# Optimization experiments

Measured on AMD Instinct MI355X. Metric: run time of the kernel, lower is better.

The kernel has to match this reference:

```python
import jax, jax.numpy as jnp
import numpy as np

T, B, N, C, H, D = 4, 8, 1024, 512, 8, 64
EPS = 1e-5


def setup_inputs() -> dict:
    key = jax.random.key(0)
    ks = jax.random.split(key, 16)
    d = {"x": jax.random.normal(ks[0], (T, B, N, C), jnp.float32)}
    for i, nm in enumerate(["q", "k", "v", "p"]):
        kW, kmu, kvar = jax.random.split(ks[1 + i], 3)
        d[f"W{nm}"] = jax.random.normal(kW, (C, C), jnp.float32) * 0.02
        d[f"b{nm}"] = jnp.zeros((C,), jnp.float32)
        d[f"g{nm}"] = jnp.ones((C,), jnp.float32)
        d[f"beta{nm}"] = jnp.zeros((C,), jnp.float32)
        d[f"mu{nm}"] = jax.random.normal(kmu, (C,), jnp.float32) * 0.1
        d[f"var{nm}"] = jax.random.uniform(kvar, (C,), jnp.float32, 0.5, 1.5)
    return d


def _lin_bn(z, W, b, g, beta, mu, var):
    # nn.Linear over channel dim, then eval-mode BatchNorm1d per channel
    y = jnp.einsum('tbnc,dc->tbnd', z, W) + b
    return (y - mu) * (g * jax.lax.rsqrt(var + EPS)) + beta


def _to_heads(z):
    # (t,b,n,c) -> (t,b,h,n,d)
    return z.reshape(T, B, N, H, D).transpose(0, 1, 3, 2, 4)


def reference(x, Wq, bq, gq, betaq, muq, varq,
              Wk, bk, gk, betak, muk, vark,
              Wv, bv, gv, betav, muv, varv,
              Wp, bp, gp, betap, mup, varp):
    q = _to_heads(_lin_bn(x, Wq, bq, gq, betaq, muq, varq))
    k = _to_heads(_lin_bn(x, Wk, bk, gk, betak, muk, vark))
    v = _to_heads(_lin_bn(x, Wv, bv, gv, betav, muv, varv))
    # attention_linear variant: kv = (k^T @ v) / N ; y = q @ kv
    kv = jnp.einsum('tbhnd,tbhne->tbhde', k, v) / float(N)  # (t,b,h,d,d)
    y = jnp.einsum('tbhnd,tbhde->tbhne', q, kv)             # (t,b,h,n,d)
    y = y.transpose(0, 1, 3, 2, 4).reshape(T, B, N, C)
    return _lin_bn(y, Wp, bp, gp, betap, mup, varp)
```

## Files before the change

kernel.cpp:

```cpp
#include <hip/hip_runtime.h>

#define T_ 4
#define B_ 8
#define N_ 1024
#define C_ 512
#define H_ 8
#define D_ 64
#define M_ (T_*B_*N_)
#define TB_ (T_*B_)

typedef __bf16 bf16;
typedef __bf16 bf16x4 __attribute__((ext_vector_type(4)));
typedef __bf16 bf16x8 __attribute__((ext_vector_type(8)));
typedef float f32x4 __attribute__((ext_vector_type(4)));

__device__ __forceinline__ void gload16(const void* g, void* l) {
  __builtin_amdgcn_global_load_lds(
      (const __attribute__((address_space(1))) void*)g,
      (__attribute__((address_space(3))) void*)l, 16, 0, 0);
}

struct PtrPack { const float* p[24]; };

__global__ __launch_bounds__(256)
void prep_all(PtrPack pk, bf16* __restrict__ WB, float* __restrict__ BS) {
  const int mat = blockIdx.x >> 9, d = blockIdx.x & 511;
  const float* W    = pk.p[6*mat + 0];
  const float* b    = pk.p[6*mat + 1];
  const float* g    = pk.p[6*mat + 2];
  const float* beta = pk.p[6*mat + 3];
  const float* mu   = pk.p[6*mat + 4];
  const float* var  = pk.p[6*mat + 5];
  float s = g[d] * rsqrtf(var[d] + 1e-5f);
  if (threadIdx.x == 0) BS[mat*512 + d] = (b[d] - mu[d]) * s + beta[d];
  bf16* Wout = WB + (size_t)mat * 262144 + (size_t)d * 512;
  for (int c = threadIdx.x; c < 512; c += 256)
    Wout[c] = (bf16)(W[(size_t)d * 512 + c] * s);
}

__global__ __launch_bounds__(256)
void prep_wqT(const float* __restrict__ W, const float* __restrict__ g,
              const float* __restrict__ var, bf16* __restrict__ WqT) {
  const int di = blockIdx.x >> 3, ci = blockIdx.x & 7;
  const int t = threadIdx.x;
  __shared__ float lds[64][65];
  const int rgrp = t >> 4, k = t & 15;
#pragma unroll
  for (int p = 0; p < 4; p++) {
    int r = p * 16 + rgrp;
    int d = di * 64 + r;
    float s = g[d] * rsqrtf(var[d] + 1e-5f);
    float4 v = *(const float4*)(W + (size_t)d * 512 + ci * 64 + k * 4);
    lds[r][k*4+0] = v.x * s; lds[r][k*4+1] = v.y * s;
    lds[r][k*4+2] = v.z * s; lds[r][k*4+3] = v.w * s;
  }
  __syncthreads();
#pragma unroll
  for (int p = 0; p < 16; p++) {
    int c = p * 4 + (t >> 6), dd = t & 63;
    WqT[(size_t)(ci*64 + c) * 512 + di*64 + dd] = (bf16)lds[dd][c];
  }
}

__global__ __launch_bounds__(256)
void cvt_x_t(const float* __restrict__ x, bf16* __restrict__ xb,
             bf16* __restrict__ xT, float* __restrict__ spart) {
  const int bid = blockIdx.x;
  const int tb = bid >> 7, nc = (bid >> 3) & 15, cc = bid & 7;
  const int t = threadIdx.x;
  __shared__ float lds[64][65];
  __shared__ float sred[16][64];
  const float* xbase = x + (size_t)tb * 524288 + (size_t)nc * 64 * 512 + cc * 64;
  bf16* xbb = xb + (size_t)tb * 524288 + (size_t)nc * 64 * 512 + cc * 64;
  bf16* xTb = xT + (size_t)tb * 524288 + (size_t)(cc * 64) * 1024 + nc * 64;
  const int rgrp = t >> 4, k = t & 15;
  float s0 = 0, s1 = 0, s2 = 0, s3 = 0;
#pragma unroll
  for (int p = 0; p < 4; p++) {
    int r = p * 16 + rgrp;
    float4 v = *(const float4*)(xbase + (size_t)r * 512 + k * 4);
    bf16x4 o; o[0]=(bf16)v.x; o[1]=(bf16)v.y; o[2]=(bf16)v.z; o[3]=(bf16)v.w;
    *(bf16x4*)(xbb + (size_t)r * 512 + k * 4) = o;
    lds[r][k*4+0]=v.x; lds[r][k*4+1]=v.y; lds[r][k*4+2]=v.z; lds[r][k*4+3]=v.w;
    s0 += v.x; s1 += v.y; s2 += v.z; s3 += v.w;
  }
  sred[rgrp][k*4+0]=s0; sred[rgrp][k*4+1]=s1; sred[rgrp][k*4+2]=s2; sred[rgrp][k*4+3]=s3;
  __syncthreads();
#pragma unroll
  for (int p = 0; p < 16; p++) {
    int c = p * 4 + (t >> 6), n = t & 63;
    xTb[(size_t)c * 1024 + n] = (bf16)lds[n][c];
  }
  if (t < 64) {
    float tot = 0;
#pragma unroll
    for (int rg = 0; rg < 16; rg++) tot += sred[rg][t];
    spart[(size_t)((tb*8 + cc)*16 + nc) * 64 + t] = tot;
  }
}

__global__ __launch_bounds__(512)
void ksvs(const bf16* __restrict__ WB, const float* __restrict__ spart,
          float* __restrict__ ksv) {
  const int tb = blockIdx.x, m = blockIdx.y;
  const int c = threadIdx.x, cc = c >> 6, cl = c & 63;
  __shared__ float sl[512];
  float tot = 0;
#pragma unroll
  for (int ncf = 0; ncf < 16; ncf++)
    tot += spart[(size_t)((tb*8 + cc)*16 + ncf) * 64 + cl];
  sl[c] = tot;
  __syncthreads();
  const bf16* Wrow = WB + (size_t)(m + 1) * 262144 + (size_t)c * 512;
  float acc = 0;
  for (int k = 0; k < 512; k += 8) {
    bf16x8 wv = *(const bf16x8*)(Wrow + k);
#pragma unroll
    for (int i = 0; i < 8; i++) acc += (float)wv[i] * sl[k + i];
  }
  ksv[m * 16384 + tb * 512 + c] = acc;
}

template <int NKT, int MTILES, bool BF16OUT, bool BIAS>
__global__ __launch_bounds__(256)
void gemm_n(const bf16* __restrict__ Abase, size_t Astr,
            const bf16* __restrict__ Btbase, size_t Btstr,
            const float* __restrict__ BSb, const float* __restrict__ cpart,
            bf16* __restrict__ ob, float* __restrict__ of, size_t Ostr) {
  constexpr int K = NKT * 64;
  constexpr int PERB = MTILES * 4;
  const int bid = blockIdx.x;
  const int xcd = bid & 7, j9 = bid >> 3;
  const int bat = xcd + 8 * (j9 / PERB);
  const int tile = j9 % PERB;
  const int mi = tile >> 2, ni = tile & 3;
  const bf16* A = Abase + (size_t)bat * Astr;
  const bf16* Bt = Btbase + (size_t)bat * Btstr;
  const int m0 = mi * 64, n0 = ni * 128;
  __shared__ __align__(16) bf16 As[64][64];
  __shared__ __align__(16) bf16 Bs[128][64];
  const int tid = threadIdx.x, w = tid >> 6, l = tid & 63;
  const int wm = w >> 1, wn = w & 1;
  const int lr = l & 15, lq = l >> 4, l7 = l & 7, lh = l >> 3;
  const int srcc = (l7 ^ lh) * 8;
  f32x4 acc[2][4] = {};
  for (int kt = 0; kt < NKT; kt++) {
#pragma unroll
    for (int i = 0; i < 2; i++) {
      int rb = w * 16 + i * 8;
      gload16(A + (size_t)(m0 + rb + lh) * K + kt * 64 + srcc, &As[rb][0]);
    }
#pragma unroll
    for (int i = 0; i < 4; i++) {
      int rb = w * 32 + i * 8;
      gload16(Bt + (size_t)(n0 + rb + lh) * K + kt * 64 + srcc, &Bs[rb][0]);
    }
    __syncthreads();
    bf16x8 af[2][2], bv[4][2];
#pragma unroll
    for (int f = 0; f < 2; f++) {
      int ra = wm * 32 + f * 16 + lr;
#pragma unroll
      for (int s = 0; s < 2; s++)
        af[f][s] = *(const bf16x8*)&As[ra][((s*4+lq) ^ (ra & 7)) * 8];
    }
#pragma unroll
    for (int f = 0; f < 4; f++) {
      int rb2 = wn * 64 + f * 16 + lr;
#pragma unroll
      for (int s = 0; s < 2; s++)
        bv[f][s] = *(const bf16x8*)&Bs[rb2][((s*4+lq) ^ (rb2 & 7)) * 8];
    }
#pragma unroll
    for (int mt = 0; mt < 2; mt++)
#pragma unroll
      for (int nt = 0; nt < 4; nt++)
#pragma unroll
        for (int s = 0; s < 2; s++)
          acc[mt][nt] = __builtin_amdgcn_mfma_f32_16x16x32_bf16(
              af[mt][s], bv[nt][s], acc[mt][nt], 0, 0, 0);
    __syncthreads();
  }

  float bja[4];
  if constexpr (BIAS) {
#pragma unroll
    for (int nt = 0; nt < 4; nt++) {
      int j = n0 + wn * 64 + nt * 16 + lr;
      float bj = BSb[1536 + j];
#pragma unroll
      for (int h = 0; h < 8; h++)
        bj += cpart[(size_t)(bat * 8 + h) * 512 + j];
      bja[nt] = bj;
    }
  }
#pragma unroll
  for (int mt = 0; mt < 2; mt++)
#pragma unroll
    for (int nt = 0; nt < 4; nt++) {
      int j = n0 + wn * 64 + nt * 16 + lr;
      size_t mrow = (size_t)m0 + wm * 32 + mt * 16 + lq * 4;
#pragma unroll
      for (int r = 0; r < 4; r++) {
        if constexpr (BF16OUT)
          ob[(size_t)bat * Ostr + (mrow + r) * 512 + j] = (bf16)acc[mt][nt][r];
        else
          of[(size_t)bat * Ostr + (mrow + r) * 512 + j] =
              acc[mt][nt][r] + (BIAS ? bja[nt] : 0.f);
      }
    }
}

__global__ __launch_bounds__(256)
void kvz(const bf16* __restrict__ KGb, const bf16* __restrict__ WB,
         const float* __restrict__ BS, const float* __restrict__ ksv,
         bf16* __restrict__ ZT, float* __restrict__ cpart) {
  const int gid = blockIdx.x, tb = gid >> 3, h = gid & 7;
  const int t = threadIdx.x, w = t >> 6, l = t & 63;
  const int lr = l & 15, lq = l >> 4;
  __shared__ __align__(16) char lds[65536 + 65536 + 8192];
  bf16* bufA = (bf16*)lds;
  bf16* bufV = (bf16*)(lds + 65536);
  bf16* kvb  = (bf16*)(lds + 131072);

#pragma unroll
  for (int i = 0; i < 16; i++) {
    int r = i * 4 + w;
    gload16(KGb + (size_t)tb * 262144 + (size_t)(64*h + r) * 512 + ((l ^ (r & 7)) * 8),
            bufA + r * 512);
    gload16(WB + 2u * 262144 + (size_t)(64*h + r) * 512 + ((l ^ (r & 7)) * 8),
            bufV + r * 512);
  }
  __syncthreads();

  f32x4 acc2[4][4] = {};
#pragma unroll
  for (int ks = 0; ks < 4; ks++) {
    int gch = w * 16 + ks * 4 + lq;
    bf16x8 af2[4], bv2[4];
#pragma unroll
    for (int mf = 0; mf < 4; mf++) {
      int d = mf * 16 + lr;
      af2[mf] = *(const bf16x8*)&bufA[d * 512 + ((gch ^ (d & 7)) * 8)];
    }
#pragma unroll
    for (int nf = 0; nf < 4; nf++) {
      int e = nf * 16 + lr;
      bv2[nf] = *(const bf16x8*)&bufV[e * 512 + ((gch ^ (e & 7)) * 8)];
    }
#pragma unroll
    for (int mf = 0; mf < 4; mf++)
#pragma unroll
      for (int nf = 0; nf < 4; nf++)
        acc2[mf][nf] = __builtin_amdgcn_mfma_f32_16x16x32_bf16(
            af2[mf], bv2[nf], acc2[mf][nf], 0, 0, 0);
  }
  __syncthreads();

  float* part = (float*)lds + w * 4096;
#pragma unroll
  for (int mf = 0; mf < 4; mf++)
#pragma unroll
    for (int nf = 0; nf < 4; nf++)
#pragma unroll
      for (int r = 0; r < 4; r++) {
        int d = mf * 16 + lq * 4 + r, e = nf * 16 + lr;
        part[d * 64 + e] = acc2[mf][nf][r];
      }
  __syncthreads();
  {
    const float inv = 1.f / 1024.f;
    const float* pb = (const float*)lds;
#pragma unroll
    for (int jj = 0; jj < 16; jj++) {
      int flat = jj * 256 + t, d = flat >> 6, e = flat & 63;
      float s = pb[flat] + pb[4096 + flat] + pb[8192 + flat] + pb[12288 + flat];
      float ksh = ksv[tb * 512 + 64*h + d];
      float vsh = ksv[16384 + tb * 512 + 64*h + e];
      float bkh = BS[512 + 64*h + d];
      float bvh = BS[1024 + 64*h + e];
      float kv = (s + ksh * bvh + bkh * vsh) * inv + bkh * bvh;
      kvb[d * 64 + (((e >> 3) ^ (d & 7)) * 8 + (e & 7))] = (bf16)kv;
    }
  }
  __syncthreads();

#pragma unroll
  for (int i = 0; i < 16; i++) {
    int rb = i * 32 + w * 8;
    int r = rb + (l >> 3);
    gload16(WB + 3u * 262144 + (size_t)r * 512 + 64*h + (((l & 7) ^ (r & 7)) * 8),
            bufA + rb * 64);
  }
  __syncthreads();

  f32x4 acc3[4][8] = {};
#pragma unroll
  for (int s = 0; s < 2; s++) {
    bf16x8 af3[4];
#pragma unroll
    for (int mf = 0; mf < 4; mf++) {
      int d = mf * 16 + lr;
      af3[mf] = *(const bf16x8*)&kvb[d * 64 + (((s*4+lq) ^ (d & 7)) * 8)];
    }
#pragma unroll
    for (int nf = 0; nf < 8; nf++) {
      int jj = w * 128 + nf * 16 + lr;
      bf16x8 b3 = *(const bf16x8*)&bufA[jj * 64 + (((s*4+lq) ^ (jj & 7)) * 8)];
#pragma unroll
      for (int mf = 0; mf < 4; mf++)
        acc3[mf][nf] = __builtin_amdgcn_mfma_f32_16x16x32_bf16(
            af3[mf], b3, acc3[mf][nf], 0, 0, 0);
    }
  }

  bf16* zbase = ZT + (size_t)tb * 262144 + 64*h;
#pragma unroll
  for (int nf = 0; nf < 8; nf++) {
    int jj = w * 128 + nf * 16 + lr;
    float cp = 0.f;
#pragma unroll
    for (int mf = 0; mf < 4; mf++) {
      bf16x4 o;
#pragma unroll
      for (int r = 0; r < 4; r++) {
        o[r] = (bf16)acc3[mf][nf][r];
        cp += acc3[mf][nf][r] * BS[64*h + mf*16 + lq*4 + r];
      }
      *(bf16x4*)(zbase + (size_t)jj * 512 + mf * 16 + lq * 4) = o;
    }
    cp += __shfl_xor(cp, 16);
    cp += __shfl_xor(cp, 32);
    if (lq == 0) cpart[(size_t)(tb * 8 + h) * 512 + jj] = cp;
  }
}

extern "C" void kernel_launch(void* const* d_in, const int* in_sizes, int n_in,
                              void* d_out, int out_size, void* d_ws, size_t ws_size,
                              hipStream_t stream) {
  const float* x = (const float*)d_in[0];
  char* ws = (char*)d_ws;
  bf16*  xb    = (bf16*)(ws + 0);
  bf16*  xT    = (bf16*)(ws + 33554432);
  bf16*  Gb    = (bf16*)(ws + 67108864);
  bf16*  KGb   = (bf16*)(ws + 83886080);
  bf16*  ZT    = (bf16*)(ws + 100663296);
  bf16*  VT    = (bf16*)(ws + 117440512);
  bf16*  WB    = (bf16*)(ws + 134217728);
  bf16*  WqT   = (bf16*)(ws + 136314880);
  float* BS    = (float*)(ws + 136839168);
  float* ksv   = (float*)(ws + 136847360);
  float* cpart = (float*)(ws + 136978432);
  float* spart = (float*)(ws + 137502720);
  (void)in_sizes; (void)n_in; (void)out_size; (void)ws_size;

  PtrPack pk;
  for (int i = 0; i < 24; i++) pk.p[i] = (const float*)d_in[1 + i];

  prep_all<<<2048, 256, 0, stream>>>(pk, WB, BS);
  prep_wqT<<<64, 256, 0, stream>>>((const float*)d_in[1], (const float*)d_in[3],
                                   (const float*)d_in[6], WqT);
  cvt_x_t<<<4096, 256, 0, stream>>>(x, xb, xT, spart);
  ksvs<<<dim3(32, 2), 512, 0, stream>>>(WB, spart, ksv);
  gemm_n<16, 8, true, false><<<1024, 256, 0, stream>>>(
      xT, 524288, xT, 524288, nullptr, nullptr, Gb, nullptr, 262144);
  gemm_n<8, 8, true, false><<<1024, 256, 0, stream>>>(
      WB + 262144, 0, Gb, 262144, nullptr, nullptr, KGb, nullptr, 262144);
  kvz<<<256, 256, 0, stream>>>(KGb, WB, BS, ksv, ZT, cpart);
  gemm_n<8, 8, true, false><<<1024, 256, 0, stream>>>(
      ZT, 262144, WqT, 0, nullptr, nullptr, VT, nullptr, 262144);
  gemm_n<8, 16, false, true><<<2048, 256, 0, stream>>>(
      xb, 524288, VT, 262144, BS, cpart, nullptr, (float*)d_out, 524288);
}
```

Before: 144.2 us.

## Exploit Gram symmetry, fuse ksvs into Gram kernel, merge prep kernels

Computes only the upper-triangular tiles of the symmetric x^T x Gram matrix (20 of 32 tiles per batch) and writes each tile plus its transpose through LDS. The kernel also runs the ksv reduction in extra blocks, and the two weight-prep kernels are merged into one launch. The aim is to cut the Gram GEMM work and remove launch overhead. It also adds a minimum-occupancy hint of 6 to gemm_n, which may force register spills.

```diff
diff --git a/kernel.cpp b/kernel.cpp
--- a/kernel.cpp
+++ b/kernel.cpp
@@ -23,27 +23,30 @@
 struct PtrPack { const float* p[24]; };
 
 __global__ __launch_bounds__(256)
-void prep_all(PtrPack pk, bf16* __restrict__ WB, float* __restrict__ BS) {
-  const int mat = blockIdx.x >> 9, d = blockIdx.x & 511;
-  const float* W    = pk.p[6*mat + 0];
-  const float* b    = pk.p[6*mat + 1];
-  const float* g    = pk.p[6*mat + 2];
-  const float* beta = pk.p[6*mat + 3];
-  const float* mu   = pk.p[6*mat + 4];
-  const float* var  = pk.p[6*mat + 5];
-  float s = g[d] * rsqrtf(var[d] + 1e-5f);
-  if (threadIdx.x == 0) BS[mat*512 + d] = (b[d] - mu[d]) * s + beta[d];
-  bf16* Wout = WB + (size_t)mat * 262144 + (size_t)d * 512;
-  for (int c = threadIdx.x; c < 512; c += 256)
-    Wout[c] = (bf16)(W[(size_t)d * 512 + c] * s);
-}
-
-__global__ __launch_bounds__(256)
-void prep_wqT(const float* __restrict__ W, const float* __restrict__ g,
-              const float* __restrict__ var, bf16* __restrict__ WqT) {
-  const int di = blockIdx.x >> 3, ci = blockIdx.x & 7;
+void prep_m(PtrPack pk, bf16* __restrict__ WB, float* __restrict__ BS,
+            bf16* __restrict__ WqT) {
   const int t = threadIdx.x;
+  if (blockIdx.x < 2048) {
+    const int mat = blockIdx.x >> 9, d = blockIdx.x & 511;
+    const float* W    = pk.p[6*mat + 0];
+    const float* b    = pk.p[6*mat + 1];
+    const float* g    = pk.p[6*mat + 2];
+    const float* beta = pk.p[6*mat + 3];
+    const float* mu   = pk.p[6*mat + 4];
+    const float* var  = pk.p[6*mat + 5];
+    float s = g[d] * rsqrtf(var[d] + 1e-5f);
+    if (t == 0) BS[mat*512 + d] = (b[d] - mu[d]) * s + beta[d];
+    bf16* Wout = WB + (size_t)mat * 262144 + (size_t)d * 512;
+    for (int c = t; c < 512; c += 256)
+      Wout[c] = (bf16)(W[(size_t)d * 512 + c] * s);
+    return;
+  }
+  const int e = blockIdx.x - 2048;
+  const int di = e >> 3, ci = e & 7;
   __shared__ float lds[64][65];
+  const float* W = pk.p[0];
+  const float* g = pk.p[2];
+  const float* var = pk.p[5];
   const int rgrp = t >> 4, k = t & 15;
 #pragma unroll
   for (int p = 0; p < 4; p++) {
@@ -99,30 +102,130 @@
   }
 }
 
-__global__ __launch_bounds__(512)
-void ksvs(const bf16* __restrict__ WB, const float* __restrict__ spart,
-          float* __restrict__ ksv) {
-  const int tb = blockIdx.x, m = blockIdx.y;
-  const int c = threadIdx.x, cc = c >> 6, cl = c & 63;
-  __shared__ float sl[512];
-  float tot = 0;
-#pragma unroll
-  for (int ncf = 0; ncf < 16; ncf++)
-    tot += spart[(size_t)((tb*8 + cc)*16 + ncf) * 64 + cl];
-  sl[c] = tot;
-  __syncthreads();
-  const bf16* Wrow = WB + (size_t)(m + 1) * 262144 + (size_t)c * 512;
-  float acc = 0;
-  for (int k = 0; k < 512; k += 8) {
-    bf16x8 wv = *(const bf16x8*)(Wrow + k);
-#pragma unroll
-    for (int i = 0; i < 8; i++) acc += (float)wv[i] * sl[k + i];
-  }
-  ksv[m * 16384 + tb * 512 + c] = acc;
+__global__ __launch_bounds__(256)
+void gram_ksvs(const bf16* __restrict__ xT, const bf16* __restrict__ WB,
+               const float* __restrict__ spart, bf16* __restrict__ Gb,
+               float* __restrict__ ksv) {
+  const int t = threadIdx.x;
+  __shared__ __align__(16) char smem[24576];
+  if (blockIdx.x >= 640) {
+    const int e = blockIdx.x - 640, tb = e >> 1, m = e & 1;
+    float* sl = (float*)smem;
+#pragma unroll
+    for (int half = 0; half < 2; half++) {
+      int c = t + half * 256, cc = c >> 6, cl = c & 63;
+      float tot = 0;
+#pragma unroll
+      for (int ncf = 0; ncf < 16; ncf++)
+        tot += spart[(size_t)((tb*8 + cc)*16 + ncf) * 64 + cl];
+      sl[c] = tot;
+    }
+    __syncthreads();
+#pragma unroll
+    for (int half = 0; half < 2; half++) {
+      int d = t + half * 256;
+      const bf16* Wrow = WB + (size_t)(m + 1) * 262144 + (size_t)d * 512;
+      float acc = 0;
+      for (int k = 0; k < 512; k += 8) {
+        bf16x8 wv = *(const bf16x8*)(Wrow + k);
+#pragma unroll
+        for (int i = 0; i < 8; i++) acc += (float)wv[i] * sl[k + i];
+      }
+      ksv[m * 16384 + tb * 512 + d] = acc;
+    }
+    return;
+  }
+  constexpr int K = 1024;
+  const int bid = blockIdx.x;
+  const int xcd = bid & 7, j9 = bid >> 3;
+  const int bat = xcd + 8 * (j9 / 20);
+  const int tile = j9 % 20;
+  int mi, ni;
+  if (tile < 8)       { mi = tile;          ni = 0; }
+  else if (tile < 14) { mi = tile - 8 + 2;  ni = 1; }
+  else if (tile < 18) { mi = tile - 14 + 4; ni = 2; }
+  else                { mi = tile - 18 + 6; ni = 3; }
+  const bf16* A = xT + (size_t)bat * 524288;
+  const int m0 = mi * 64, n0 = ni * 128;
+  bf16* As = (bf16*)smem;
+  bf16* Bs = (bf16*)(smem + 8192);
+  const int w = t >> 6, l = t & 63;
+  const int wm = w >> 1, wn = w & 1;
+  const int lr = l & 15, lq = l >> 4, l7 = l & 7, lh = l >> 3;
+  const int srcc = (l7 ^ lh) * 8;
+  f32x4 acc[2][4] = {};
+  for (int kt = 0; kt < 16; kt++) {
+#pragma unroll
+    for (int i = 0; i < 2; i++) {
+      int rb = w * 16 + i * 8;
+      gload16(A + (size_t)(m0 + rb + lh) * K + kt * 64 + srcc, &As[rb * 64]);
+    }
+#pragma unroll
+    for (int i = 0; i < 4; i++) {
+      int rb = w * 32 + i * 8;
+      gload16(A + (size_t)(n0 + rb + lh) * K + kt * 64 + srcc, &Bs[rb * 64]);
+    }
+    __syncthreads();
+    bf16x8 af[2][2], bv[4][2];
+#pragma unroll
+    for (int f = 0; f < 2; f++) {
+      int ra = wm * 32 + f * 16 + lr;
+#pragma unroll
+      for (int s = 0; s < 2; s++)
+        af[f][s] = *(const bf16x8*)&As[ra * 64 + (((s*4+lq) ^ (ra & 7)) * 8)];
+    }
+#pragma unroll
+    for (int f = 0; f < 4; f++) {
+      int rb2 = wn * 64 + f * 16 + lr;
+#pragma unroll
+      for (int s = 0; s < 2; s++)
+        bv[f][s] = *(const bf16x8*)&Bs[rb2 * 64 + (((s*4+lq) ^ (rb2 & 7)) * 8)];
+    }
+#pragma unroll
+    for (int mt = 0; mt < 2; mt++)
+#pragma unroll
+      for (int nt = 0; nt < 4; nt++)
+#pragma unroll
+        for (int s = 0; s < 2; s++)
+          acc[mt][nt] = __builtin_amdgcn_mfma_f32_16x16x32_bf16(
+              af[mt][s], bv[nt][s], acc[mt][nt], 0, 0, 0);
+    __syncthreads();
+  }
+  bf16* ob = Gb + (size_t)bat * 262144;
+#pragma unroll
+  for (int mt = 0; mt < 2; mt++)
+#pragma unroll
+    for (int nt = 0; nt < 4; nt++) {
+      int j = n0 + wn * 64 + nt * 16 + lr;
+      size_t mrow = (size_t)m0 + wm * 32 + mt * 16 + lq * 4;
+#pragma unroll
+      for (int r = 0; r < 4; r++)
+        ob[(mrow + r) * 512 + j] = (bf16)acc[mt][nt][r];
+    }
+  bf16* TB = (bf16*)smem;
+#pragma unroll
+  for (int mt = 0; mt < 2; mt++)
+#pragma unroll
+    for (int nt = 0; nt < 4; nt++) {
+      int a = wn * 64 + nt * 16 + lr;
+#pragma unroll
+      for (int r = 0; r < 4; r++) {
+        int b = wm * 32 + mt * 16 + lq * 4 + r;
+        TB[(a * 64 + b) ^ ((a & 7) << 3)] = (bf16)acc[mt][nt][r];
+      }
+    }
+  __syncthreads();
+  const int rowa = t >> 1, half = t & 1;
+#pragma unroll
+  for (int i = 0; i < 4; i++) {
+    int c8 = half * 4 + i;
+    bf16x8 v = *(const bf16x8*)&TB[(rowa * 64 + c8 * 8) ^ ((rowa & 7) << 3)];
+    *(bf16x8*)(ob + (size_t)(n0 + rowa) * 512 + m0 + c8 * 8) = v;
+  }
 }
 
 template <int NKT, int MTILES, bool BF16OUT, bool BIAS>
-__global__ __launch_bounds__(256)
+__global__ __launch_bounds__(256, 6)
 void gemm_n(const bf16* __restrict__ Abase, size_t Astr,
             const bf16* __restrict__ Btbase, size_t Btstr,
             const float* __restrict__ BSb, const float* __restrict__ cpart,
@@ -357,13 +460,9 @@
   PtrPack pk;
   for (int i = 0; i < 24; i++) pk.p[i] = (const float*)d_in[1 + i];
 
-  prep_all<<<2048, 256, 0, stream>>>(pk, WB, BS);
-  prep_wqT<<<64, 256, 0, stream>>>((const float*)d_in[1], (const float*)d_in[3],
-                                   (const float*)d_in[6], WqT);
+  prep_m<<<2112, 256, 0, stream>>>(pk, WB, BS, WqT);
   cvt_x_t<<<4096, 256, 0, stream>>>(x, xb, xT, spart);
-  ksvs<<<dim3(32, 2), 512, 0, stream>>>(WB, spart, ksv);
-  gemm_n<16, 8, true, false><<<1024, 256, 0, stream>>>(
-      xT, 524288, xT, 524288, nullptr, nullptr, Gb, nullptr, 262144);
+  gram_ksvs<<<704, 256, 0, stream>>>(xT, WB, spart, Gb, ksv);
   gemm_n<8, 8, true, false><<<1024, 256, 0, stream>>>(
       WB + 262144, 0, Gb, 262144, nullptr, nullptr, KGb, nullptr, 262144);
   kvz<<<256, 256, 0, stream>>>(KGb, WB, BS, ksv, ZT, cpart);
```

New measurement: 134.6 us. 1.07x faster.
